# Optimization experiments

Measured on AMD Instinct MI355X. Metric: run time of the kernel, lower is better.

## Reference

```python
import jax, jax.numpy as jnp
import numpy as np

NOTRACK_BOX = jnp.array([-1.0, -1.0, -1.0, -1.0], dtype=jnp.float32)
ROI_SIZE = 7


def make_boxes(key, B, N):
    k1, k2 = jax.random.split(key)
    lo = jax.random.uniform(k1, (B, N, 2)) * 0.5            # (ymin, xmin)
    sz = jax.random.uniform(k2, (B, N, 2)) * 0.45 + 0.05    # box extent
    hi = jnp.minimum(lo + sz, 1.0)
    boxes = jnp.concatenate([lo, hi], axis=-1)               # [B,N,4] ymin,xmin,ymax,xmax
    # mark last 2 slots per batch as empty (NOTRACK_BOX)
    boxes = boxes.at[:, -2:, :].set(-1.0)
    return boxes


def setup_inputs() -> dict:
    key = jax.random.key(0)
    ks = jax.random.split(key, 6)
    B, H, W, N, C, D = 16, 512, 512, 16, 256, 256
    images = jax.random.normal(ks[0], (B, H, W, 3), dtype=jnp.float32)
    bboxes = make_boxes(ks[1], B, N)
    conv_w = jax.random.normal(ks[2], (16, 16, 3, C), dtype=jnp.float32) * 0.05
    conv_b = jnp.zeros((C,), dtype=jnp.float32)
    dense_w = jax.random.normal(ks[3], (C, D), dtype=jnp.float32) * (1.0 / np.sqrt(C))
    dense_b = jnp.zeros((D,), dtype=jnp.float32)
    return {"images": images, "bboxes": bboxes, "conv_w": conv_w,
            "conv_b": conv_b, "dense_w": dense_w, "dense_b": dense_b}


def backbone(images, conv_w, conv_b):
    # stride-16 conv stem: [B,512,512,3] -> [B,32,32,C]
    feat = jax.lax.conv_general_dilated(
        images, conv_w, window_strides=(16, 16), padding="VALID",
        dimension_numbers=("NHWC", "HWIO", "NHWC"))
    return jax.nn.relu(feat + conv_b)


def roi_align(bboxes, feat, size):
    # bboxes: [B,N,4] normalized (ymin,xmin,ymax,xmax); feat: [B,H,W,C]
    B, H, W, C = feat.shape
    ymin, xmin, ymax, xmax = [bboxes[..., i] for i in range(4)]  # each [B,N]
    steps = (jnp.arange(size, dtype=feat.dtype) + 0.5) / size    # [S]
    ys = ymin[..., None] + (ymax - ymin)[..., None] * steps      # [B,N,S]
    xs = xmin[..., None] + (xmax - xmin)[..., None] * steps      # [B,N,S]
    py = ys * H - 0.5
    px = xs * W - 0.5
    y0f = jnp.floor(py); x0f = jnp.floor(px)
    wy = py - y0f; wx = px - x0f                                 # [B,N,S]
    y0 = jnp.clip(y0f.astype(jnp.int32), 0, H - 1)
    y1 = jnp.clip(y0f.astype(jnp.int32) + 1, 0, H - 1)
    x0 = jnp.clip(x0f.astype(jnp.int32), 0, W - 1)
    x1 = jnp.clip(x0f.astype(jnp.int32) + 1, 0, W - 1)
    N, S = y0.shape[1], size
    def grid(yi, xi):  # [B,N,S] x [B,N,S] -> [B,N,S,S] index grids
        return (jnp.broadcast_to(yi[:, :, :, None], (B, N, S, S)),
                jnp.broadcast_to(xi[:, :, None, :], (B, N, S, S)))
    gather = jax.vmap(lambda f, yy, xx: f[yy, xx])  # per-batch fancy gather
    def corner(yi, xi):
        yy, xx = grid(yi, xi)
        return gather(feat, yy, xx)                              # [B,N,S,S,C]
    w00 = ((1 - wy)[:, :, :, None] * (1 - wx)[:, :, None, :])[..., None]
    w01 = ((1 - wy)[:, :, :, None] * wx[:, :, None, :])[..., None]
    w10 = (wy[:, :, :, None] * (1 - wx)[:, :, None, :])[..., None]
    w11 = (wy[:, :, :, None] * wx[:, :, None, :])[..., None]
    return (w00 * corner(y0, x0) + w01 * corner(y0, x1)
            + w10 * corner(y1, x0) + w11 * corner(y1, x1))        # [B,N,S,S,C]


def reference(images, bboxes, conv_w, conv_b, dense_w, dense_b):
    bboxes = jax.lax.stop_gradient(bboxes)
    feat = backbone(images, conv_w, conv_b)                      # [B,32,32,C]
    roi = roi_align(bboxes, feat, ROI_SIZE)                      # [B,N,S,S,C]
    obj = jnp.mean(roi, axis=(-3, -2))                           # [B,N,C] (mean aggregate)
    is_non_empty = jnp.any(bboxes != NOTRACK_BOX, axis=-1, keepdims=True)
    obj = jnp.where(is_non_empty, obj, jnp.zeros_like(obj))
    return obj @ dense_w + dense_b                               # [B,N,D]
```

## Files before the change

### kernel.cpp

```cpp
#include <hip/hip_runtime.h>
#include <hip/hip_bf16.h>

typedef __attribute__((ext_vector_type(8))) short bf16x8;
typedef __attribute__((ext_vector_type(4))) float f32x4;
typedef __attribute__((ext_vector_type(4))) int i32x4;

__device__ inline unsigned int pack_bf2(float a, float b) {
    unsigned int ua = __builtin_bit_cast(unsigned int, a);
    unsigned int ub = __builtin_bit_cast(unsigned int, b);
    ua = (ua + 0x7fffu + ((ua >> 16) & 1u)) >> 16;
    ub = (ub + 0x7fffu + ((ub >> 16) & 1u)) >> 16;
    return (ub << 16) | (ua & 0xffffu);
}
__device__ inline unsigned short f2bf1(float a) {
    unsigned int u = __builtin_bit_cast(unsigned int, a);
    u = (u + 0x7fffu + ((u >> 16) & 1u)) >> 16;
    return (unsigned short)u;
}
__device__ inline float bf2f(unsigned short u) {
    return __builtin_bit_cast(float, ((unsigned int)u) << 16);
}

__global__ void pack_w_kernel(const float* __restrict__ conv_w, i32x4* __restrict__ bpack) {
    int t = blockIdx.x * 256 + threadIdx.x;
    int lane = t & 63;
    int g = t >> 6;
    int nt = g / 24, ks = g - nt * 24;
    int k0 = ks * 32 + ((lane >> 4) << 3);
    int n  = nt * 16 + (lane & 15);
    const float* src = conv_w + (size_t)k0 * 256 + n;
    float v[8];
#pragma unroll
    for (int j = 0; j < 8; ++j) v[j] = src[(size_t)j * 256];
    i32x4 o;
    o.x = pack_bf2(v[0], v[1]);
    o.y = pack_bf2(v[2], v[3]);
    o.z = pack_bf2(v[4], v[5]);
    o.w = pack_bf2(v[6], v[7]);
    bpack[t] = o;
}

__global__ __launch_bounds__(512) void conv_kernel(
    const float* __restrict__ images,
    const i32x4* __restrict__ bpack,
    const float* __restrict__ conv_b,
    unsigned short* __restrict__ featB) {
    __shared__ short ldsA[2][32 * 200];

    const int tid  = threadIdx.x;
    const int lane = tid & 63;
    const int w    = tid >> 6;
    const int l15  = lane & 15;
    const int lg   = lane >> 4;

    const int g = blockIdx.x;
    const int b = g >> 5, ii = g & 31;

    const int sr = tid >> 7;
    const int tc = tid & 127;
    const float* rowb = images + (size_t)(b * 512 + ii * 16 + sr) * 1536 + tc * 4;

    int widx[3];
#pragma unroll
    for (int p = 0; p < 3; ++p) {
        int f0 = tc * 4 + p * 512;
        int j = f0 / 48;
        int off = f0 - 48 * j;
        widx[p] = j * 200 + sr * 48 + off;
    }

    float bias[2];
#pragma unroll
    for (int sub = 0; sub < 2; ++sub)
        bias[sub] = conv_b[w * 32 + sub * 16 + l15];

    const i32x4* bp = bpack + (size_t)(2 * w * 24) * 64 + lane;

    f32x4 acc[2][2] = {};
    f32x4 sA[3], sB[3];

    {
        f32x4 t0[3];
#pragma unroll
        for (int p = 0; p < 3; ++p) t0[p] = *(const f32x4*)(rowb + p * 512);
#pragma unroll
        for (int p = 0; p < 3; ++p) sB[p] = *(const f32x4*)(rowb + 6144 + p * 512);
#pragma unroll
        for (int p = 0; p < 3; ++p) {
            int2 v;
            v.x = pack_bf2(t0[p].x, t0[p].y);
            v.y = pack_bf2(t0[p].z, t0[p].w);
            *(int2*)(&ldsA[0][widx[p]]) = v;
        }
    }
    asm volatile("s_waitcnt lgkmcnt(0)" ::: "memory");
    __builtin_amdgcn_s_barrier();
    __builtin_amdgcn_sched_barrier(0);

#pragma unroll
    for (int rc = 0; rc < 4; ++rc) {
        i32x4 Bc[2][6];
#pragma unroll
        for (int sub = 0; sub < 2; ++sub)
#pragma unroll
        for (int s = 0; s < 6; ++s)
            Bc[sub][s] = bp[(size_t)(sub * 24 + rc * 6 + s) * 64];
        __builtin_amdgcn_sched_barrier(0);
        if (rc == 0) {
#pragma unroll
            for (int p = 0; p < 3; ++p) sA[p] = *(const f32x4*)(rowb + 2 * 6144 + p * 512);
        }
        if (rc == 1) {
#pragma unroll
            for (int p = 0; p < 3; ++p) sB[p] = *(const f32x4*)(rowb + 3 * 6144 + p * 512);
        }
        const short* bufA = &ldsA[rc & 1][0];
#pragma unroll
        for (int s = 0; s < 6; ++s) {
            bf16x8 aF0 = *(const bf16x8*)(&bufA[l15 * 200 + s * 32 + lg * 8]);
            bf16x8 aF1 = *(const bf16x8*)(&bufA[(16 + l15) * 200 + s * 32 + lg * 8]);
#pragma unroll
            for (int sub = 0; sub < 2; ++sub) {
                bf16x8 bF = __builtin_bit_cast(bf16x8, Bc[sub][s]);
                acc[0][sub] = __builtin_amdgcn_mfma_f32_16x16x32_bf16(aF0, bF, acc[0][sub], 0, 0, 0);
                acc[1][sub] = __builtin_amdgcn_mfma_f32_16x16x32_bf16(aF1, bF, acc[1][sub], 0, 0, 0);
            }
        }
        __builtin_amdgcn_sched_barrier(0);
        if (rc < 3) {
            short* dst = &ldsA[(rc + 1) & 1][0];
            if ((rc & 1) == 0) {
#pragma unroll
                for (int p = 0; p < 3; ++p) {
                    int2 v;
                    v.x = pack_bf2(sB[p].x, sB[p].y);
                    v.y = pack_bf2(sB[p].z, sB[p].w);
                    *(int2*)(&dst[widx[p]]) = v;
                }
            } else {
#pragma unroll
                for (int p = 0; p < 3; ++p) {
                    int2 v;
                    v.x = pack_bf2(sA[p].x, sA[p].y);
                    v.y = pack_bf2(sA[p].z, sA[p].w);
                    *(int2*)(&dst[widx[p]]) = v;
                }
            }
        }
        asm volatile("s_waitcnt lgkmcnt(0)" ::: "memory");
        __builtin_amdgcn_s_barrier();
        __builtin_amdgcn_sched_barrier(0);
    }

    const int m0 = g * 32;
#pragma unroll
    for (int mt = 0; mt < 2; ++mt)
#pragma unroll
    for (int sub = 0; sub < 2; ++sub)
#pragma unroll
    for (int r = 0; r < 4; ++r) {
        int m = m0 + mt * 16 + lg * 4 + r;
        int n = w * 32 + sub * 16 + l15;
        float v = acc[mt][sub][r] + bias[sub];
        featB[(size_t)m * 256 + n] = f2bf1(fmaxf(v, 0.f));
    }
}

__global__ __launch_bounds__(1024) void roi_dense_kernel(
    const float* __restrict__ bboxes,
    const unsigned short* __restrict__ featB,
    const float* __restrict__ dense_w,
    const float* __restrict__ dense_b,
    float* __restrict__ out) {
    __shared__ int   offs[4][49];
    __shared__ float wts[4][49];
    __shared__ float part[1024];
    __shared__ float objv[256];

    const int bn = blockIdx.x;
    const int b  = bn >> 4;
    const int tid = threadIdx.x;
    const int c  = tid & 255;
    const int h  = tid >> 8;

    const float4 box = *(const float4*)(bboxes + (size_t)bn * 4);
    bool empty = (box.x == -1.f) & (box.y == -1.f) & (box.z == -1.f) & (box.w == -1.f);
    if (empty) {
        if (tid < 256) out[(size_t)bn * 256 + tid] = dense_b[tid];
        return;
    }

    if (tid < 49) {
        int sy = tid / 7, sx = tid - sy * 7;
        float py = (box.x + (box.z - box.x) * ((sy + 0.5f) * (1.0f / 7.0f))) * 32.f - 0.5f;
        float px = (box.y + (box.w - box.y) * ((sx + 0.5f) * (1.0f / 7.0f))) * 32.f - 0.5f;
        float y0f = floorf(py), x0f = floorf(px);
        float wy = py - y0f, wx = px - x0f;
        int y0 = min(max((int)y0f, 0), 31);
        int y1 = min(max((int)y0f + 1, 0), 31);
        int x0 = min(max((int)x0f, 0), 31);
        int x1 = min(max((int)x0f + 1, 0), 31);
        offs[0][tid] = (y0 * 32 + x0) * 256;
        offs[1][tid] = (y0 * 32 + x1) * 256;
        offs[2][tid] = (y1 * 32 + x0) * 256;
        offs[3][tid] = (y1 * 32 + x1) * 256;
        wts[0][tid] = (1.f - wy) * (1.f - wx);
        wts[1][tid] = (1.f - wy) * wx;
        wts[2][tid] = wy * (1.f - wx);
        wts[3][tid] = wy * wx;
    }
    __syncthreads();

    const unsigned short* fb = featB + (size_t)b * (1024 * 256) + c;
    float a0 = 0.f, a1 = 0.f, a2 = 0.f, a3 = 0.f;
    for (int s = h; s < 49; s += 4) {
        a0 += wts[0][s] * bf2f(fb[offs[0][s]]);
        a1 += wts[1][s] * bf2f(fb[offs[1][s]]);
        a2 += wts[2][s] * bf2f(fb[offs[2][s]]);
        a3 += wts[3][s] * bf2f(fb[offs[3][s]]);
    }
    part[tid] = (a0 + a1) + (a2 + a3);
    __syncthreads();
    if (tid < 256)
        objv[tid] = ((part[tid] + part[tid + 256]) + (part[tid + 512] + part[tid + 768]))
                    * (1.f / 49.f);
    __syncthreads();

    const float* dwp = dense_w + (size_t)(h * 64) * 256 + c;
    const float* ov  = &objv[h * 64];
    float d0 = 0.f, d1 = 0.f;
#pragma unroll 8
    for (int kk = 0; kk < 64; kk += 2) {
        d0 += ov[kk]     * dwp[(size_t)kk * 256];
        d1 += ov[kk + 1] * dwp[(size_t)(kk + 1) * 256];
    }
    part[tid] = d0 + d1;
    __syncthreads();
    if (tid < 256)
        out[(size_t)bn * 256 + tid] =
            ((part[tid] + part[tid + 256]) + (part[tid + 512] + part[tid + 768]))
            + dense_b[tid];
}

extern "C" void kernel_launch(void* const* d_in, const int* in_sizes, int n_in,
                              void* d_out, int out_size, void* d_ws, size_t ws_size,
                              hipStream_t stream) {
    const float* images  = (const float*)d_in[0];
    const float* bboxes  = (const float*)d_in[1];
    const float* conv_w  = (const float*)d_in[2];
    const float* conv_b  = (const float*)d_in[3];
    const float* dense_w = (const float*)d_in[4];
    const float* dense_b = (const float*)d_in[5];
    float* out = (float*)d_out;

    char* ws = (char*)d_ws;
    i32x4* bpack = (i32x4*)ws;
    unsigned short* featB = (unsigned short*)(ws + 512 * 1024);

    pack_w_kernel<<<96, 256, 0, stream>>>(conv_w, bpack);
    conv_kernel<<<512, 512, 0, stream>>>(images, bpack, conv_b, featB);
    roi_dense_kernel<<<256, 1024, 0, stream>>>(bboxes, featB, dense_w, dense_b, out);
}
```

Measured before the change: 34.57 us.

## Prefetch all image rows and double-buffer weight fragments in registers for conv GEMM

Restructures the conv-stem GEMM prologue so all four image row chunks are loaded into registers up front, and weight fragments are double-buffered in two register sets (BA/BB). The next weight chunk is issued right after the MFMAs of the current chunk instead of at the start of each iteration. The goal is to hide global load latency behind MFMA work rather than stalling at the top of each chunk. The cost is higher register pressure, which may lower occupancy or cause spills.

```diff
diff --git a/kernel.cpp b/kernel.cpp
--- a/kernel.cpp
+++ b/kernel.cpp
@@ -77,21 +77,37 @@
     const i32x4* bp = bpack + (size_t)(2 * w * 24) * 64 + lane;
 
     f32x4 acc[2][2] = {};
-    f32x4 sA[3], sB[3];
-
-    {
-        f32x4 t0[3];
-#pragma unroll
-        for (int p = 0; p < 3; ++p) t0[p] = *(const f32x4*)(rowb + p * 512);
-#pragma unroll
-        for (int p = 0; p < 3; ++p) sB[p] = *(const f32x4*)(rowb + 6144 + p * 512);
-#pragma unroll
-        for (int p = 0; p < 3; ++p) {
-            int2 v;
-            v.x = pack_bf2(t0[p].x, t0[p].y);
-            v.y = pack_bf2(t0[p].z, t0[p].w);
-            *(int2*)(&ldsA[0][widx[p]]) = v;
-        }
+    f32x4 s0[3], s1[3], s2[3], s3[3];
+    i32x4 BA[2][6], BB[2][6];
+
+#pragma unroll
+    for (int sub = 0; sub < 2; ++sub)
+#pragma unroll
+    for (int s = 0; s < 6; ++s)
+        BA[sub][s] = bp[(size_t)(sub * 24 + s) * 64];
+    __builtin_amdgcn_sched_barrier(0);
+#pragma unroll
+    for (int p = 0; p < 3; ++p) s0[p] = *(const f32x4*)(rowb + p * 512);
+    __builtin_amdgcn_sched_barrier(0);
+#pragma unroll
+    for (int sub = 0; sub < 2; ++sub)
+#pragma unroll
+    for (int s = 0; s < 6; ++s)
+        BB[sub][s] = bp[(size_t)(sub * 24 + 6 + s) * 64];
+    __builtin_amdgcn_sched_barrier(0);
+#pragma unroll
+    for (int p = 0; p < 3; ++p) s1[p] = *(const f32x4*)(rowb + 6144 + p * 512);
+#pragma unroll
+    for (int p = 0; p < 3; ++p) s2[p] = *(const f32x4*)(rowb + 2 * 6144 + p * 512);
+#pragma unroll
+    for (int p = 0; p < 3; ++p) s3[p] = *(const f32x4*)(rowb + 3 * 6144 + p * 512);
+    __builtin_amdgcn_sched_barrier(0);
+#pragma unroll
+    for (int p = 0; p < 3; ++p) {
+        int2 v;
+        v.x = pack_bf2(s0[p].x, s0[p].y);
+        v.y = pack_bf2(s0[p].z, s0[p].w);
+        *(int2*)(&ldsA[0][widx[p]]) = v;
     }
     asm volatile("s_waitcnt lgkmcnt(0)" ::: "memory");
     __builtin_amdgcn_s_barrier();
@@ -99,21 +115,6 @@
 
 #pragma unroll
     for (int rc = 0; rc < 4; ++rc) {
-        i32x4 Bc[2][6];
-#pragma unroll
-        for (int sub = 0; sub < 2; ++sub)
-#pragma unroll
-        for (int s = 0; s < 6; ++s)
-            Bc[sub][s] = bp[(size_t)(sub * 24 + rc * 6 + s) * 64];
-        __builtin_amdgcn_sched_barrier(0);
-        if (rc == 0) {
-#pragma unroll
-            for (int p = 0; p < 3; ++p) sA[p] = *(const f32x4*)(rowb + 2 * 6144 + p * 512);
-        }
-        if (rc == 1) {
-#pragma unroll
-            for (int p = 0; p < 3; ++p) sB[p] = *(const f32x4*)(rowb + 3 * 6144 + p * 512);
-        }
         const short* bufA = &ldsA[rc & 1][0];
 #pragma unroll
         for (int s = 0; s < 6; ++s) {
@@ -121,30 +122,53 @@
             bf16x8 aF1 = *(const bf16x8*)(&bufA[(16 + l15) * 200 + s * 32 + lg * 8]);
 #pragma unroll
             for (int sub = 0; sub < 2; ++sub) {
-                bf16x8 bF = __builtin_bit_cast(bf16x8, Bc[sub][s]);
+                bf16x8 bF = __builtin_bit_cast(bf16x8,
+                    ((rc & 1) == 0) ? BA[sub][s] : BB[sub][s]);
                 acc[0][sub] = __builtin_amdgcn_mfma_f32_16x16x32_bf16(aF0, bF, acc[0][sub], 0, 0, 0);
                 acc[1][sub] = __builtin_amdgcn_mfma_f32_16x16x32_bf16(aF1, bF, acc[1][sub], 0, 0, 0);
             }
         }
         __builtin_amdgcn_sched_barrier(0);
-        if (rc < 3) {
-            short* dst = &ldsA[(rc + 1) & 1][0];
-            if ((rc & 1) == 0) {
-#pragma unroll
-                for (int p = 0; p < 3; ++p) {
-                    int2 v;
-                    v.x = pack_bf2(sB[p].x, sB[p].y);
-                    v.y = pack_bf2(sB[p].z, sB[p].w);
-                    *(int2*)(&dst[widx[p]]) = v;
-                }
-            } else {
-#pragma unroll
-                for (int p = 0; p < 3; ++p) {
-                    int2 v;
-                    v.x = pack_bf2(sA[p].x, sA[p].y);
-                    v.y = pack_bf2(sA[p].z, sA[p].w);
-                    *(int2*)(&dst[widx[p]]) = v;
-                }
+        if (rc == 0) {
+#pragma unroll
+            for (int sub = 0; sub < 2; ++sub)
+#pragma unroll
+            for (int s = 0; s < 6; ++s)
+                BA[sub][s] = bp[(size_t)(sub * 24 + 12 + s) * 64];
+        }
+        if (rc == 1) {
+#pragma unroll
+            for (int sub = 0; sub < 2; ++sub)
+#pragma unroll
+            for (int s = 0; s < 6; ++s)
+                BB[sub][s] = bp[(size_t)(sub * 24 + 18 + s) * 64];
+        }
+        __builtin_amdgcn_sched_barrier(0);
+        if (rc == 0) {
+#pragma unroll
+            for (int p = 0; p < 3; ++p) {
+                int2 v;
+                v.x = pack_bf2(s1[p].x, s1[p].y);
+                v.y = pack_bf2(s1[p].z, s1[p].w);
+                *(int2*)(&ldsA[1][widx[p]]) = v;
+            }
+        }
+        if (rc == 1) {
+#pragma unroll
+            for (int p = 0; p < 3; ++p) {
+                int2 v;
+                v.x = pack_bf2(s2[p].x, s2[p].y);
+                v.y = pack_bf2(s2[p].z, s2[p].w);
+                *(int2*)(&ldsA[0][widx[p]]) = v;
+            }
+        }
+        if (rc == 2) {
+#pragma unroll
+            for (int p = 0; p < 3; ++p) {
+                int2 v;
+                v.x = pack_bf2(s3[p].x, s3[p].y);
+                v.y = pack_bf2(s3[p].z, s3[p].w);
+                *(int2*)(&ldsA[1][widx[p]]) = v;
             }
         }
         asm volatile("s_waitcnt lgkmcnt(0)" ::: "memory");
```

Result: slower. 37.13 us (+7.4%).
